# Performance work log

Measured on AMD Instinct MI355X. Metric: run time of the kernel, lower is better.

## Reference

```python
import jax, jax.numpy as jnp
import numpy as np
from itertools import product


def _gen_exps(num_vars, degree):
    return [e for e in product(range(degree + 1), repeat=num_vars) if sum(e) <= degree]

EXP_W = _gen_exps(7, 3)  # 120 terms
EXP_B = _gen_exps(3, 3)  # 20 terms
EXP_M = _gen_exps(5, 3)  # 56 terms (+1 diagonal coeff)


def _powers(x, exps):
    return {e: x ** e for e in exps}


def setup_inputs() -> dict:
    key = jax.random.key(0)
    ks = jax.random.split(key, 12)
    B, Din, Dout = 65536, 64, 64
    return {
        'x1': jax.random.normal(ks[0], (B, Din), jnp.float32),
        's1': jax.random.normal(ks[1], (B, Dout), jnp.float32),
        'y1': jax.random.normal(ks[2], (B, Dout), jnp.float32),
        'x2': jax.random.normal(ks[3], (B, Din), jnp.float32),
        's2': jax.random.normal(ks[4], (B, Dout), jnp.float32),
        'y2': jax.random.normal(ks[5], (B, Dout), jnp.float32),
        'w': jax.random.normal(ks[6], (Dout, Din), jnp.float32) * 0.1,
        'b': jax.random.normal(ks[7], (Dout,), jnp.float32) * 0.1,
        'm': jax.random.normal(ks[8], (Dout, Dout), jnp.float32) * 0.1,
        'params_w': jax.random.normal(ks[9], (len(EXP_W),), jnp.float32) * 0.1,
        'params_b': jax.random.normal(ks[10], (len(EXP_B),), jnp.float32) * 0.1,
        'params_m': jax.random.normal(ks[11], (len(EXP_M) + 1,), jnp.float32) * 0.1,
    }


def _dw(x1, s1, y1, x2, s2, y2, w, params_w):
    px1 = _powers(x1, {e[0] for e in EXP_W})
    ps1 = _powers(s1, {e[1] for e in EXP_W})
    py1 = _powers(y1, {e[2] for e in EXP_W})
    px2 = _powers(x2, {e[3] for e in EXP_W})
    ps2 = _powers(s2, {e[4] for e in EXP_W})
    py2 = _powers(y2, {e[5] for e in EXP_W})
    pw = _powers(w, {e[6] for e in EXP_W})
    inv_b = 1.0 / x1.shape[0]
    delta_w = jnp.zeros_like(w)
    for i, e in enumerate(EXP_W):
        y_term = ps1[e[1]] * py1[e[2]] * ps2[e[4]] * py2[e[5]]  # [B, Dout]
        x_term = px1[e[0]] * px2[e[3]]                          # [B, Din]
        delta_w = delta_w + (params_w[i] * inv_b) * (y_term.T @ x_term) * pw[e[6]]
    return delta_w  # bound=None (identity), l2_reg=0


def _db(y1, y2, b, params_b):
    py1 = _powers(y1, {e[0] for e in EXP_B})
    py2 = _powers(y2, {e[1] for e in EXP_B})
    pb = _powers(b, {e[2] for e in EXP_B})
    inv_b = 1.0 / y1.shape[0]
    delta_b = jnp.zeros_like(b)
    for i, e in enumerate(EXP_B):
        delta_b = delta_b + (params_b[i] * inv_b) * jnp.sum(py1[e[0]] * py2[e[1]], axis=0) * pb[e[2]]
    return delta_b


def _dm(y1, y2, m, params_m):
    ey1 = {e[0] for e in EXP_M} | {e[1] for e in EXP_M}
    ey2 = {e[2] for e in EXP_M} | {e[3] for e in EXP_M}
    py1 = _powers(y1, ey1)
    py2 = _powers(y2, ey2)
    pm = _powers(m, {e[4] for e in EXP_M})
    inv_b = 1.0 / y1.shape[0]
    delta_m = jnp.zeros_like(m)
    for i, e in enumerate(EXP_M):
        left = py1[e[1]] * py2[e[3]]   # [B, Dout]
        right = py1[e[0]] * py2[e[2]]  # [B, Dout]
        delta_m = delta_m + (params_m[i] * inv_b) * (left.T @ right) * pm[e[4]]
    delta_m = delta_m + params_m[-1] * jnp.eye(m.shape[0], dtype=m.dtype)
    return delta_m


def reference(x1, s1, y1, x2, s2, y2, w, b, m, params_w, params_b, params_m):
    delta_w = _dw(x1, s1, y1, x2, s2, y2, w, params_w)
    delta_b = _db(y1, y2, b, params_b)
    delta_m = _dm(y1, y2, m, params_m)
    return delta_w, delta_b, delta_m
```

## Files before the change

kernel.cpp:

```cpp
#include <hip/hip_runtime.h>
#include <type_traits>
#include <stdint.h>

#define DEV __device__ __forceinline__

typedef float f32x4 __attribute__((ext_vector_type(4)));
typedef short bf16x8 __attribute__((ext_vector_type(8)));
typedef unsigned short u16;
typedef u16 u16x4 __attribute__((ext_vector_type(4)));

static constexpr int BTOT = 65536;
static constexpr int KB   = 64;
static constexpr int NCHT = BTOT / KB;
static constexpr int NG   = 56;
static constexpr int NCOLSUM = 45;
static constexpr float INVB = 1.0f / (float)BTOT;

static constexpr int NWIN   = 64;
static constexpr int NBLK_C = 64;
static constexpr int NBLK_R = 256;
static constexpr int GRID   = 8*NWIN;

struct Col {
  int nslot, np, nsplit, nb;
  int8_t sexp[10][6];
  int8_t pa[16], pb[16];
  int16_t gout[16];
  uint8_t ldmask;
};

struct Tables {
  int nW, nB, nM, nA, nX;
  int8_t expw[120][7];
  int8_t expb[20][3];
  int8_t expm[56][5];
  int8_t am[35][4];
  int8_t xm[10][2];
  Col col[4];
  int8_t wtype[120]; int16_t widx[120]; int8_t wpow[120];
  int8_t mtype[56];  int16_t midx[56];  int8_t mpow[56];
  int16_t bcol[20];  int8_t bpow[20];
  int err, gcount;
};

constexpr int aidf(const Tables& t,int a,int b,int c,int d){
  for(int i=0;i<t.nA;i++)
    if(t.am[i][0]==a&&t.am[i][1]==b&&t.am[i][2]==c&&t.am[i][3]==d) return i;
  return -1;
}
constexpr int xidf(const Tables& t,int a,int b){
  for(int i=0;i<t.nX;i++) if(t.xm[i][0]==a&&t.xm[i][1]==b) return i;
  return -1;
}

constexpr Tables makeTables(){
  Tables t{};
  t.err = 0;
  t.nW=0;
  for(int e0=0;e0<4;e0++)for(int e1=0;e1<4;e1++)for(int e2=0;e2<4;e2++)
  for(int e3=0;e3<4;e3++)for(int e4=0;e4<4;e4++)for(int e5=0;e5<4;e5++)
  for(int e6=0;e6<4;e6++) if(e0+e1+e2+e3+e4+e5+e6<=3){
    t.expw[t.nW][0]=(int8_t)e0; t.expw[t.nW][1]=(int8_t)e1; t.expw[t.nW][2]=(int8_t)e2;
    t.expw[t.nW][3]=(int8_t)e3; t.expw[t.nW][4]=(int8_t)e4; t.expw[t.nW][5]=(int8_t)e5;
    t.expw[t.nW][6]=(int8_t)e6; t.nW++;
  }
  t.nB=0;
  for(int e0=0;e0<4;e0++)for(int e1=0;e1<4;e1++)for(int e2=0;e2<4;e2++)
    if(e0+e1+e2<=3){ t.expb[t.nB][0]=(int8_t)e0; t.expb[t.nB][1]=(int8_t)e1; t.expb[t.nB][2]=(int8_t)e2; t.nB++; }
  t.nM=0;
  for(int e0=0;e0<4;e0++)for(int e1=0;e1<4;e1++)for(int e2=0;e2<4;e2++)
  for(int e3=0;e3<4;e3++)for(int e4=0;e4<4;e4++)
    if(e0+e1+e2+e3+e4<=3){
      t.expm[t.nM][0]=(int8_t)e0; t.expm[t.nM][1]=(int8_t)e1; t.expm[t.nM][2]=(int8_t)e2;
      t.expm[t.nM][3]=(int8_t)e3; t.expm[t.nM][4]=(int8_t)e4; t.nM++;
    }
  t.nA=0;
  for(int a=0;a<4;a++)for(int b=0;b<4;b++)for(int c=0;c<4;c++)for(int d=0;d<4;d++)
    if(a+b+c+d<=3){ t.am[t.nA][0]=(int8_t)a; t.am[t.nA][1]=(int8_t)b; t.am[t.nA][2]=(int8_t)c; t.am[t.nA][3]=(int8_t)d; t.nA++; }
  t.nX=0;
  for(int a=0;a<4;a++)for(int b=0;b<4;b++)
    if(a+b<=3){ t.xm[t.nX][0]=(int8_t)a; t.xm[t.nX][1]=(int8_t)b; t.nX++; }

  int wslot[35][10]; int mslot[10][10];
  for(int i=0;i<35;i++)for(int j=0;j<10;j++) wslot[i][j]=-1;
  for(int i=0;i<10;i++)for(int j=0;j<10;j++) mslot[i][j]=-1;

  int slot=0;

  {
    Col& c = t.col[0]; c.nslot=5; c.nsplit=1; c.nb=NBLK_C;
    int ye[5][2] = {{0,1},{1,0},{0,2},{1,1},{2,0}};
    int xmid[5] = {0,0,0,0,0};
    for(int s=0;s<5;s++){
      c.sexp[s][0]=0; c.sexp[s][1]=(int8_t)ye[s][0]; c.sexp[s][2]=0;
      c.sexp[s][3]=(int8_t)ye[s][1]; c.sexp[s][4]=0; c.sexp[s][5]=0;
      xmid[s]=xidf(t, ye[s][0], ye[s][1]);
      if(xmid[s]<0) t.err+=1;
    }
    int p=0;
    for(int L=0;L<2;L++)for(int R=0;R<5;R++){
      c.pa[p]=(int8_t)L; c.pb[p]=(int8_t)R; c.gout[p]=(int16_t)slot;
      mslot[xmid[L]][xmid[R]]=slot; slot++; p++;
    }
    for(int L=2;L<5;L++)for(int R=0;R<2;R++){
      c.pa[p]=(int8_t)L; c.pb[p]=(int8_t)R; c.gout[p]=(int16_t)slot;
      mslot[xmid[L]][xmid[R]]=slot; slot++; p++;
    }
    c.np=p;
    if(p!=16) t.err+=1;
  }
  for(int wc=0; wc<2; wc++){
    Col& c = t.col[1+wc]; c.nslot=10; c.nsplit=1; c.nb=NBLK_C;
    int ae[5][2] = {{1,0},{0,1},{2,0},{1,1},{0,2}};
    int xe[5][2] = {{0,1},{1,0},{0,2},{1,1},{2,0}};
    int amid[5]={0,0,0,0,0}, xmidb[5]={0,0,0,0,0};
    for(int s=0;s<5;s++){
      for(int q=0;q<6;q++) c.sexp[s][q]=0;
      if(wc==0){ c.sexp[s][0]=(int8_t)ae[s][0]; c.sexp[s][1]=(int8_t)ae[s][1];
                 amid[s]=aidf(t, ae[s][0], ae[s][1], 0, 0); }
      else     { c.sexp[s][2]=(int8_t)ae[s][0]; c.sexp[s][3]=(int8_t)ae[s][1];
                 amid[s]=aidf(t, 0, 0, ae[s][0], ae[s][1]); }
      if(amid[s]<0) t.err+=1;
      for(int q=0;q<6;q++) c.sexp[5+s][q]=0;
      c.sexp[5+s][4]=(int8_t)xe[s][0]; c.sexp[5+s][5]=(int8_t)xe[s][1];
      xmidb[s]=xidf(t, xe[s][0], xe[s][1]);
      if(xmidb[s]<0) t.err+=1;
    }
    int p=0;
    for(int a=0;a<2;a++)for(int b=0;b<5;b++){
      c.pa[p]=(int8_t)a; c.pb[p]=(int8_t)(5+b); c.gout[p]=(int16_t)slot;
      wslot[amid[a]][xmidb[b]]=slot; slot++; p++;
    }
    for(int a=2;a<5;a++)for(int b=0;b<2;b++){
      c.pa[p]=(int8_t)a; c.pb[p]=(int8_t)(5+b); c.gout[p]=(int16_t)slot;
      wslot[amid[a]][xmidb[b]]=slot; slot++; p++;
    }
    c.np=p;
    if(p!=16) t.err+=1;
  }
  {
    Col& c = t.col[3]; c.nslot=6; c.nsplit=2; c.nb=NBLK_C;
    int ae4[4][4] = {{1,0,1,0},{1,0,0,1},{0,1,1,0},{0,1,0,1}};
    int xe[2][2] = {{0,1},{1,0}};
    int amid[4]={0,0,0,0}, xmidb[2]={0,0};
    for(int s=0;s<4;s++){
      c.sexp[s][0]=(int8_t)ae4[s][0]; c.sexp[s][1]=(int8_t)ae4[s][1];
      c.sexp[s][2]=(int8_t)ae4[s][2]; c.sexp[s][3]=(int8_t)ae4[s][3];
      c.sexp[s][4]=0; c.sexp[s][5]=0;
      amid[s]=aidf(t, ae4[s][0], ae4[s][1], ae4[s][2], ae4[s][3]);
      if(amid[s]<0) t.err+=1;
    }
    for(int s=0;s<2;s++){
      for(int q=0;q<6;q++) c.sexp[4+s][q]=0;
      c.sexp[4+s][4]=(int8_t)xe[s][0]; c.sexp[4+s][5]=(int8_t)xe[s][1];
      xmidb[s]=xidf(t, xe[s][0], xe[s][1]);
      if(xmidb[s]<0) t.err+=1;
    }
    int p=0;
    for(int a=0;a<4;a++)for(int b=0;b<2;b++){
      c.pa[p]=(int8_t)a; c.pb[p]=(int8_t)(4+b); c.gout[p]=(int16_t)slot;
      wslot[amid[a]][xmidb[b]]=slot; slot++; p++;
    }
    c.np=p;
    if(p!=8) t.err+=1;
  }
  t.gcount=slot;
  if(slot!=NG) t.err+=1;

  for(int ci=0; ci<4; ci++){
    unsigned m=0;
    for(int s=0;s<t.col[ci].nslot;s++)
      for(int v=0;v<6;v++) if(t.col[ci].sexp[s][v]>0) m |= (1u<<v);
    t.col[ci].ldmask=(uint8_t)m;
  }

  for(int i=0;i<t.nW;i++){
    const int8_t* e=t.expw[i];
    bool u0=(e[0]==0&&e[3]==0);
    bool v0=(e[1]==0&&e[2]==0&&e[4]==0&&e[5]==0);
    t.wpow[i]=e[6];
    if(u0){ t.wtype[i]=1; t.widx[i]=(int16_t)aidf(t,e[1],e[2],e[4],e[5]); }
    else if(v0){ t.wtype[i]=2; t.widx[i]=(int16_t)xidf(t,e[0],e[3]); }
    else {
      int s=wslot[aidf(t,e[1],e[2],e[4],e[5])][xidf(t,e[0],e[3])];
      if(s<0) t.err+=1;
      t.wtype[i]=0; t.widx[i]=(int16_t)s;
    }
  }
  for(int i=0;i<t.nM;i++){
    const int8_t* e=t.expm[i];
    bool L0=(e[1]==0&&e[3]==0), R0=(e[0]==0&&e[2]==0);
    t.mpow[i]=e[4];
    if(L0){ t.mtype[i]=2; t.midx[i]=(int16_t)aidf(t,0,e[0],0,e[2]); }
    else if(R0){ t.mtype[i]=1; t.midx[i]=(int16_t)aidf(t,0,e[1],0,e[3]); }
    else {
      int s=mslot[xidf(t,e[1],e[3])][xidf(t,e[0],e[2])];
      if(s<0) t.err+=1;
      t.mtype[i]=0; t.midx[i]=(int16_t)s;
    }
  }
  for(int i=0;i<t.nB;i++){
    const int8_t* e=t.expb[i];
    t.bcol[i]=(int16_t)aidf(t,0,e[0],0,e[1]); t.bpow[i]=e[2];
  }
  return t;
}

constexpr Tables TB = makeTables();
static_assert(TB.err==0 && TB.gcount==56, "table build failed");
static_assert(TB.nW==120 && TB.nB==20 && TB.nM==56 && TB.nA==35 && TB.nX==10, "enumeration mismatch");

template<int N, typename F>
DEV void sunroll(F&& f){
  if constexpr (N > 0){
    sunroll<N-1>(static_cast<F&&>(f));
    f(std::integral_constant<int, N-1>{});
  }
}
template<int E> DEV float ipw(float x){
  if constexpr(E==0) return 1.0f;
  else if constexpr(E==1) return x;
  else if constexpr(E==2) return x*x;
  else return x*x*x;
}
DEV u16 f2bf(float f){
  uint32_t u = __builtin_bit_cast(uint32_t, f);
  u = u + 0x7FFFu + ((u>>16)&1u);
  return (u16)(u>>16);
}

DEV bf16x8 readFrag(const u16* lds, int slot, int sb, int t, int l){
  return *(const bf16x8*)&lds[slot*4096 + ((sb*4 + t)*64 + l)*8];
}

template<int CI>
DEV void colGemm(const float* __restrict__ s1,const float* __restrict__ y1,
                 const float* __restrict__ s2,const float* __restrict__ y2,
                 const float* __restrict__ x1,const float* __restrict__ x2,
                 float* __restrict__ G, u16* lds, int tid, int bi)
{
  constexpr int NS  = TB.col[CI].nslot;
  constexpr int NSP = TB.col[CI].nsplit;
  constexpr int NDB = 4/NSP;
  constexpr int NB  = TB.col[CI].nb;
  constexpr unsigned LM = TB.col[CI].ldmask;

  const int l=tid&63, ob=(tid>>6)&3, sub=tid>>8, w=tid>>6;
  const int q = (l>>4)&3;
  const int ch = ob*16 + (l&15);
  const int bl = sub*16 + q*4;
  const int wbase = ((( (sub>>1)*4 + ob)*64) + ((sub&1)*2 + (q>>1))*16 + (l&15))*8 + (q&1)*4;

  int aslot=0,bslot=0,gsl=0,dbase=0;
  sunroll<16>([&](auto W){
    constexpr int ww = decltype(W)::value;
    if(w==ww){
      constexpr int p = ww/NSP;
      aslot = TB.col[CI].pa[p];
      bslot = TB.col[CI].pb[p];
      gsl   = TB.col[CI].gout[p];
      dbase = (ww%NSP)*2;
    }
  });

  const int c0 = (bi*NCHT)/NB, c1 = ((bi+1)*NCHT)/NB;
  f32x4 acc[4][NDB] = {};

  float raw[6][4] = {};
  float nraw[6][4] = {};

  auto issue = [&](int ck, float (&dst)[6][4]){
    const int b0 = (ck*KB + bl)*64 + ch;
    #pragma unroll
    for(int j=0;j<4;j++){
      const int off = b0 + j*64;
      if constexpr(LM&1u)  dst[0][j]=s1[off];
      if constexpr(LM&2u)  dst[1][j]=y1[off];
      if constexpr(LM&4u)  dst[2][j]=s2[off];
      if constexpr(LM&8u)  dst[3][j]=y2[off];
      if constexpr(LM&16u) dst[4][j]=x1[off];
      if constexpr(LM&32u) dst[5][j]=x2[off];
    }
  };

  issue(c0, raw);

  for(int ck=c0; ck<c1; ++ck){
    const int nk = (ck+1<c1)? ck+1 : c0;
    issue(nk, nraw);

    sunroll<NS>([&](auto S){
      constexpr int s = decltype(S)::value;
      u16x4 o4;
      #pragma unroll
      for(int j=0;j<4;j++){
        float v = ipw<TB.col[CI].sexp[s][0]>(raw[0][j])
                * ipw<TB.col[CI].sexp[s][1]>(raw[1][j])
                * ipw<TB.col[CI].sexp[s][2]>(raw[2][j])
                * ipw<TB.col[CI].sexp[s][3]>(raw[3][j])
                * ipw<TB.col[CI].sexp[s][4]>(raw[4][j])
                * ipw<TB.col[CI].sexp[s][5]>(raw[5][j]);
        o4[j]=f2bf(v);
      }
      *(u16x4*)&lds[s*4096 + wbase] = o4;
    });

    asm volatile("s_waitcnt lgkmcnt(0)" ::: "memory");
    __builtin_amdgcn_s_barrier();
    __builtin_amdgcn_sched_barrier(0);

    #pragma unroll
    for(int sb=0; sb<2; ++sb){
      bf16x8 Af[4];
      #pragma unroll
      for(int o2=0;o2<4;o2++) Af[o2]=readFrag(lds,aslot,sb,o2,l);
      #pragma unroll
      for(int dd=0;dd<NDB;dd++){
        bf16x8 Bf=readFrag(lds,bslot,sb,dbase+dd,l);
        #pragma unroll
        for(int o2=0;o2<4;o2++)
          acc[o2][dd]=__builtin_amdgcn_mfma_f32_16x16x32_bf16(Af[o2],Bf,acc[o2][dd],0,0,0);
      }
    }

    __builtin_amdgcn_sched_barrier(0);
    __builtin_amdgcn_s_barrier();
    __builtin_amdgcn_sched_barrier(0);

    #pragma unroll
    for(int a=0;a<6;a++)
      #pragma unroll
      for(int j=0;j<4;j++) raw[a][j]=nraw[a][j];
  }

  float* dst = G + gsl*4096;
  const int r0=(l>>4)*4, cc=l&15;
  #pragma unroll
  for(int o2=0;o2<4;o2++)
    #pragma unroll
    for(int dd=0;dd<NDB;dd++)
      #pragma unroll
      for(int r=0;r<4;r++)
        atomicAdd(&dst[(o2*16+r0+r)*64 + (dbase+dd)*16+cc], acc[o2][dd][r]);
}

DEV void colRed(const float* __restrict__ s1,const float* __restrict__ y1,
                const float* __restrict__ s2,const float* __restrict__ y2,
                const float* __restrict__ x1,const float* __restrict__ x2,
                float* __restrict__ col, float* ldsF, int tid, int bi)
{
  const int ch=tid&63, g=tid>>6;
  const int c0=(bi*NCHT)/NBLK_R, c1=((bi+1)*NCHT)/NBLK_R;
  float accv[45];
  sunroll<45>([&](auto K){ accv[decltype(K)::value]=0.f; });
  for(int r=c0*KB+g; r<c1*KB; r+=16){
    const int off=r*64+ch;
    const float v0=s1[off],v1=y1[off],v2=s2[off],v3=y2[off],v4=x1[off],v5=x2[off];
    sunroll<35>([&](auto K){
      constexpr int k=decltype(K)::value;
      accv[k] += ipw<TB.am[k][0]>(v0)*ipw<TB.am[k][1]>(v1)*ipw<TB.am[k][2]>(v2)*ipw<TB.am[k][3]>(v3);
    });
    sunroll<10>([&](auto K){
      constexpr int k=decltype(K)::value;
      accv[35+k] += ipw<TB.xm[k][0]>(v4)*ipw<TB.xm[k][1]>(v5);
    });
  }
  sunroll<5>([&](auto RR){
    constexpr int rr=decltype(RR)::value;
    __syncthreads();
    sunroll<9>([&](auto Q){
      constexpr int q=decltype(Q)::value;
      ldsF[(q*16+g)*64+ch]=accv[rr*9+q];
    });
    __syncthreads();
    if(tid<576){
      const int q=tid>>6, c=tid&63;
      float s=0.f;
      #pragma unroll
      for(int gg=0; gg<16; gg++) s+=ldsF[(q*16+gg)*64+c];
      atomicAdd(&col[(rr*9+q)*64+c], s);
    }
  });
}

__global__ __launch_bounds__(1024) void k_main(
    const float* __restrict__ x1, const float* __restrict__ s1, const float* __restrict__ y1,
    const float* __restrict__ x2, const float* __restrict__ s2, const float* __restrict__ y2,
    float* __restrict__ G, float* __restrict__ col)
{
  __shared__ u16 lds[10*4096];
  const int tid = threadIdx.x;
  const int u = blockIdx.x >> 6;
  const int g = blockIdx.x & 63;
  if      (u==0) colGemm<0>(s1,y1,s2,y2,x1,x2,G,lds,tid,g);
  else if (u==1) colGemm<1>(s1,y1,s2,y2,x1,x2,G,lds,tid,g);
  else if (u==2) colGemm<2>(s1,y1,s2,y2,x1,x2,G,lds,tid,g);
  else if (u==3) colGemm<3>(s1,y1,s2,y2,x1,x2,G,lds,tid,g);
  else           colRed(s1,y1,s2,y2,x1,x2,col,(float*)lds,tid, g*4 + (u-4));
}

__global__ __launch_bounds__(256) void k_combine(
    const float* __restrict__ G, const float* __restrict__ col,
    const float* __restrict__ w, const float* __restrict__ b, const float* __restrict__ m,
    const float* __restrict__ parw, const float* __restrict__ parb, const float* __restrict__ parm,
    float* __restrict__ out)
{
  const int n = blockIdx.x*256 + threadIdx.x;
  const int o = n>>6, d = n&63;
  const float wv = w[n], mv = m[n];
  const float wp[4] = {1.f, wv, wv*wv, wv*wv*wv};
  const float mp[4] = {1.f, mv, mv*mv, mv*mv*mv};
  float aw=0.f, am=0.f;
  sunroll<120>([&](auto II){
    constexpr int i = decltype(II)::value;
    constexpr int ty = TB.wtype[i];
    constexpr int ix = TB.widx[i];
    constexpr int q  = TB.wpow[i];
    float val;
    if constexpr(ty==0) val = G[ix*4096 + n];
    else if constexpr(ty==1) val = col[ix*64 + o];
    else val = col[(35+ix)*64 + d];
    aw += parw[i] * val * wp[q];
  });
  sunroll<56>([&](auto II){
    constexpr int i = decltype(II)::value;
    constexpr int ty = TB.mtype[i];
    constexpr int ix = TB.midx[i];
    constexpr int q  = TB.mpow[i];
    float val;
    if constexpr(ty==0) val = G[ix*4096 + n];
    else if constexpr(ty==1) val = col[ix*64 + o];
    else val = col[ix*64 + d];
    am += parm[i] * val * mp[q];
  });
  aw *= INVB; am *= INVB;
  if (o==d) am += parm[56];
  out[n] = aw;
  out[4160 + n] = am;
  if (n < 64){
    const float bv = b[n];
    const float bp[4] = {1.f, bv, bv*bv, bv*bv*bv};
    float ab=0.f;
    sunroll<20>([&](auto II){
      constexpr int i = decltype(II)::value;
      constexpr int cix = TB.bcol[i];
      constexpr int q = TB.bpow[i];
      ab += parb[i] * col[cix*64 + n] * bp[q];
    });
    out[4096 + n] = ab * INVB;
  }
}

extern "C" void kernel_launch(void* const* d_in, const int* in_sizes, int n_in,
                              void* d_out, int out_size, void* d_ws, size_t ws_size,
                              hipStream_t stream)
{
  const float* x1=(const float*)d_in[0];
  const float* s1=(const float*)d_in[1];
  const float* y1=(const float*)d_in[2];
  const float* x2=(const float*)d_in[3];
  const float* s2=(const float*)d_in[4];
  const float* y2=(const float*)d_in[5];
  const float* w =(const float*)d_in[6];
  const float* b =(const float*)d_in[7];
  const float* m =(const float*)d_in[8];
  const float* parw=(const float*)d_in[9];
  const float* parb=(const float*)d_in[10];
  const float* parm=(const float*)d_in[11];

  float* G   = (float*)d_ws;
  float* col = G + NG*4096;

  hipMemsetAsync(d_ws, 0, (size_t)(NG*4096 + NCOLSUM*64)*sizeof(float), stream);
  k_main<<<GRID, 1024, 0, stream>>>(x1,s1,y1,x2,s2,y2,G,col);
  k_combine<<<16, 256, 0, stream>>>(G,col,w,b,m,parw,parb,parm,(float*)d_out);
}
```

Baseline: 108.9 us.

## Halve block size and pair GEMM products per wave to reuse fragments

Blocks shrink from 1024 to 512 threads with two blocks per CU. Each wave now computes one or two full 64x64 products, grouped by a compile-time table so that the pair shares either its A or its B fragments, instead of splitting one product across waves. Each thread loads 8 rows and writes 8-wide bf16 vectors to LDS. The column-reduction blocks are resized to 8 row groups of 256 rows each. The aim is fewer redundant LDS fragment reads, wider stores, and better occupancy, at the cost of more accumulator registers per wave (two 4x4 f32x4 sets) and a possible spill risk under the 2-block launch bound.

```diff
diff --git a/kernel.cpp b/kernel.cpp
--- a/kernel.cpp
+++ b/kernel.cpp
@@ -7,7 +7,7 @@
 typedef float f32x4 __attribute__((ext_vector_type(4)));
 typedef short bf16x8 __attribute__((ext_vector_type(8)));
 typedef unsigned short u16;
-typedef u16 u16x4 __attribute__((ext_vector_type(4)));
+typedef u16 u16x8 __attribute__((ext_vector_type(8)));
 
 static constexpr int BTOT = 65536;
 static constexpr int KB   = 64;
@@ -19,7 +19,7 @@
 static constexpr int NWIN   = 64;
 static constexpr int NBLK_C = 64;
 static constexpr int NBLK_R = 256;
-static constexpr int GRID   = 8*NWIN;
+static constexpr int GRID   = 4*NWIN + NBLK_R;
 
 struct Col {
   int nslot, np, nsplit, nb;
@@ -210,6 +210,37 @@
 static_assert(TB.err==0 && TB.gcount==56, "table build failed");
 static_assert(TB.nW==120 && TB.nB==20 && TB.nM==56 && TB.nA==35 && TB.nX==10, "enumeration mismatch");
 
+constexpr int WP1[4][8] = {
+  {0,2,5,7,4,10,12,14},
+  {0,2,5,7,4,10,12,14},
+  {0,2,5,7,4,10,12,14},
+  {0,1,2,3,4,5,6,7}
+};
+constexpr int WP2[4][8] = {
+  {1,3,6,8,9,11,13,15},
+  {1,3,6,8,9,11,13,15},
+  {1,3,6,8,9,11,13,15},
+  {-1,-1,-1,-1,-1,-1,-1,-1}
+};
+constexpr bool wpOK(){
+  for(int c=0;c<4;c++){
+    bool used[16]={};
+    for(int w=0;w<8;w++){
+      int p1=WP1[c][w], p2=WP2[c][w];
+      if(p1<0||p1>=TB.col[c].np) return false;
+      if(used[p1]) return false; used[p1]=true;
+      if(p2>=0){
+        if(p2>=TB.col[c].np) return false;
+        if(used[p2]) return false; used[p2]=true;
+        if(TB.col[c].pa[p1]!=TB.col[c].pa[p2] && TB.col[c].pb[p1]!=TB.col[c].pb[p2]) return false;
+      }
+    }
+    for(int p=0;p<TB.col[c].np;p++) if(!used[p]) return false;
+  }
+  return true;
+}
+static_assert(wpOK(), "wave pair grouping invalid");
+
 template<int N, typename F>
 DEV void sunroll(F&& f){
   if constexpr (N > 0){
@@ -231,6 +262,10 @@
 
 DEV bf16x8 readFrag(const u16* lds, int slot, int sb, int t, int l){
   return *(const bf16x8*)&lds[slot*4096 + ((sb*4 + t)*64 + l)*8];
+}
+
+DEV f32x4 mfma_(bf16x8 a, bf16x8 b, f32x4 c){
+  return __builtin_amdgcn_mfma_f32_16x16x32_bf16(a, b, c, 0, 0, 0);
 }
 
 template<int CI>
@@ -239,40 +274,23 @@
                  const float* __restrict__ x1,const float* __restrict__ x2,
                  float* __restrict__ G, u16* lds, int tid, int bi)
 {
-  constexpr int NS  = TB.col[CI].nslot;
-  constexpr int NSP = TB.col[CI].nsplit;
-  constexpr int NDB = 4/NSP;
-  constexpr int NB  = TB.col[CI].nb;
+  constexpr int NS = TB.col[CI].nslot;
   constexpr unsigned LM = TB.col[CI].ldmask;
 
-  const int l=tid&63, ob=(tid>>6)&3, sub=tid>>8, w=tid>>6;
-  const int q = (l>>4)&3;
-  const int ch = ob*16 + (l&15);
-  const int bl = sub*16 + q*4;
-  const int wbase = ((( (sub>>1)*4 + ob)*64) + ((sub&1)*2 + (q>>1))*16 + (l&15))*8 + (q&1)*4;
-
-  int aslot=0,bslot=0,gsl=0,dbase=0;
-  sunroll<16>([&](auto W){
-    constexpr int ww = decltype(W)::value;
-    if(w==ww){
-      constexpr int p = ww/NSP;
-      aslot = TB.col[CI].pa[p];
-      bslot = TB.col[CI].pb[p];
-      gsl   = TB.col[CI].gout[p];
-      dbase = (ww%NSP)*2;
-    }
-  });
-
-  const int c0 = (bi*NCHT)/NB, c1 = ((bi+1)*NCHT)/NB;
-  f32x4 acc[4][NDB] = {};
-
-  float raw[6][4] = {};
-  float nraw[6][4] = {};
-
-  auto issue = [&](int ck, float (&dst)[6][4]){
-    const int b0 = (ck*KB + bl)*64 + ch;
+  const int l = tid&63, w = tid>>6;
+  const int wbase = (((w>>2)*4 + (l>>4))*64 + (w&3)*16 + (l&15))*8;
+
+  const int c0 = bi*16, c1 = c0+16;
+  f32x4 accA[4][4] = {};
+  f32x4 accB[4][4] = {};
+
+  float raw[6][8] = {};
+  float nraw[6][8] = {};
+
+  auto issue = [&](int ck, float (&dst)[6][8]){
+    const int b0 = (ck*KB + w*8)*64 + l;
     #pragma unroll
-    for(int j=0;j<4;j++){
+    for(int j=0;j<8;j++){
       const int off = b0 + j*64;
       if constexpr(LM&1u)  dst[0][j]=s1[off];
       if constexpr(LM&2u)  dst[1][j]=y1[off];
@@ -291,37 +309,73 @@
 
     sunroll<NS>([&](auto S){
       constexpr int s = decltype(S)::value;
-      u16x4 o4;
+      u16x8 o8;
       #pragma unroll
-      for(int j=0;j<4;j++){
+      for(int j=0;j<8;j++){
         float v = ipw<TB.col[CI].sexp[s][0]>(raw[0][j])
                 * ipw<TB.col[CI].sexp[s][1]>(raw[1][j])
                 * ipw<TB.col[CI].sexp[s][2]>(raw[2][j])
                 * ipw<TB.col[CI].sexp[s][3]>(raw[3][j])
                 * ipw<TB.col[CI].sexp[s][4]>(raw[4][j])
                 * ipw<TB.col[CI].sexp[s][5]>(raw[5][j]);
-        o4[j]=f2bf(v);
+        o8[j]=f2bf(v);
       }
-      *(u16x4*)&lds[s*4096 + wbase] = o4;
+      *(u16x8*)&lds[s*4096 + wbase] = o8;
     });
 
     asm volatile("s_waitcnt lgkmcnt(0)" ::: "memory");
     __builtin_amdgcn_s_barrier();
     __builtin_amdgcn_sched_barrier(0);
 
-    #pragma unroll
-    for(int sb=0; sb<2; ++sb){
-      bf16x8 Af[4];
-      #pragma unroll
-      for(int o2=0;o2<4;o2++) Af[o2]=readFrag(lds,aslot,sb,o2,l);
-      #pragma unroll
-      for(int dd=0;dd<NDB;dd++){
-        bf16x8 Bf=readFrag(lds,bslot,sb,dbase+dd,l);
+    sunroll<8>([&](auto WW){
+      constexpr int ww = decltype(WW)::value;
+      if(w==ww){
+        constexpr int P1 = WP1[CI][ww], P2 = WP2[CI][ww];
+        constexpr int SA1 = TB.col[CI].pa[P1], SB1 = TB.col[CI].pb[P1];
         #pragma unroll
-        for(int o2=0;o2<4;o2++)
-          acc[o2][dd]=__builtin_amdgcn_mfma_f32_16x16x32_bf16(Af[o2],Bf,acc[o2][dd],0,0,0);
+        for(int sb=0; sb<2; ++sb){
+          if constexpr(P2 >= 0){
+            constexpr int SA2 = TB.col[CI].pa[P2], SB2 = TB.col[CI].pb[P2];
+            if constexpr(SA1 == SA2){
+              bf16x8 Af[4];
+              #pragma unroll
+              for(int o2=0;o2<4;o2++) Af[o2]=readFrag(lds,SA1,sb,o2,l);
+              #pragma unroll
+              for(int dd=0;dd<4;dd++){
+                bf16x8 Bf1=readFrag(lds,SB1,sb,dd,l);
+                #pragma unroll
+                for(int o2=0;o2<4;o2++) accA[o2][dd]=mfma_(Af[o2],Bf1,accA[o2][dd]);
+                bf16x8 Bf2=readFrag(lds,SB2,sb,dd,l);
+                #pragma unroll
+                for(int o2=0;o2<4;o2++) accB[o2][dd]=mfma_(Af[o2],Bf2,accB[o2][dd]);
+              }
+            } else {
+              bf16x8 Af1[4], Af2[4];
+              #pragma unroll
+              for(int o2=0;o2<4;o2++){ Af1[o2]=readFrag(lds,SA1,sb,o2,l); Af2[o2]=readFrag(lds,SA2,sb,o2,l); }
+              #pragma unroll
+              for(int dd=0;dd<4;dd++){
+                bf16x8 Bf=readFrag(lds,SB1,sb,dd,l);
+                #pragma unroll
+                for(int o2=0;o2<4;o2++) accA[o2][dd]=mfma_(Af1[o2],Bf,accA[o2][dd]);
+                #pragma unroll
+                for(int o2=0;o2<4;o2++) accB[o2][dd]=mfma_(Af2[o2],Bf,accB[o2][dd]);
+              }
+            }
+          } else {
+            bf16x8 Af[4];
+            #pragma unroll
+            for(int o2=0;o2<4;o2++) Af[o2]=readFrag(lds,SA1,sb,o2,l);
+            #pragma unroll
+            for(int dd=0;dd<4;dd++){
+              bf16x8 Bf=readFrag(lds,SB1,sb,dd,l);
+              #pragma unroll
+              for(int o2=0;o2<4;o2++) accA[o2][dd]=mfma_(Af[o2],Bf,accA[o2][dd]);
+            }
+          }
+        }
       }
-    }
+    });
 
     __builtin_amdgcn_sched_barrier(0);
     __builtin_amdgcn_s_barrier();
@@ -330,18 +384,38 @@
     #pragma unroll
     for(int a=0;a<6;a++)
       #pragma unroll
-      for(int j=0;j<4;j++) raw[a][j]=nraw[a][j];
-  }
-
-  float* dst = G + gsl*4096;
+      for(int j=0;j<8;j++) raw[a][j]=nraw[a][j];
+  }
+
   const int r0=(l>>4)*4, cc=l&15;
-  #pragma unroll
-  for(int o2=0;o2<4;o2++)
-    #pragma unroll
-    for(int dd=0;dd<NDB;dd++)
-      #pragma unroll
-      for(int r=0;r<4;r++)
-        atomicAdd(&dst[(o2*16+r0+r)*64 + (dbase+dd)*16+cc], acc[o2][dd][r]);
+  sunroll<8>([&](auto WW){
+    constexpr int ww = decltype(WW)::value;
+    if(w==ww){
+      constexpr int P1 = WP1[CI][ww], P2 = WP2[CI][ww];
+      constexpr int G1 = TB.col[CI].gout[P1];
+      {
+        float* dst = G + G1*4096;
+        #pragma unroll
+        for(int o2=0;o2<4;o2++)
+          #pragma unroll
+          for(int dd=0;dd<4;dd++)
+            #pragma unroll
+            for(int r=0;r<4;r++)
+              atomicAdd(&dst[(o2*16+r0+r)*64 + dd*16+cc], accA[o2][dd][r]);
+      }
+      if constexpr(P2 >= 0){
+        constexpr int G2 = TB.col[CI].gout[P2];
+        float* dst = G + G2*4096;
+        #pragma unroll
+        for(int o2=0;o2<4;o2++)
+          #pragma unroll
+          for(int dd=0;dd<4;dd++)
+            #pragma unroll
+            for(int r=0;r<4;r++)
+              atomicAdd(&dst[(o2*16+r0+r)*64 + dd*16+cc], accB[o2][dd][r]);
+      }
+    }
+  });
 }
 
 DEV void colRed(const float* __restrict__ s1,const float* __restrict__ y1,
@@ -349,11 +423,11 @@
                 const float* __restrict__ x1,const float* __restrict__ x2,
                 float* __restrict__ col, float* ldsF, int tid, int bi)
 {
-  const int ch=tid&63, g=tid>>6;
-  const int c0=(bi*NCHT)/NBLK_R, c1=((bi+1)*NCHT)/NBLK_R;
+  const int ch=tid&63, g8=tid>>6;
+  const int row0 = bi*256;
   float accv[45];
   sunroll<45>([&](auto K){ accv[decltype(K)::value]=0.f; });
-  for(int r=c0*KB+g; r<c1*KB; r+=16){
+  for(int r=row0+g8; r<row0+256; r+=8){
     const int off=r*64+ch;
     const float v0=s1[off],v1=y1[off],v2=s2[off],v3=y2[off],v4=x1[off],v5=x2[off];
     sunroll<35>([&](auto K){
@@ -365,38 +439,46 @@
       accv[35+k] += ipw<TB.xm[k][0]>(v4)*ipw<TB.xm[k][1]>(v5);
     });
   }
-  sunroll<5>([&](auto RR){
+  sunroll<6>([&](auto RR){
     constexpr int rr=decltype(RR)::value;
     __syncthreads();
-    sunroll<9>([&](auto Q){
+    sunroll<8>([&](auto Q){
       constexpr int q=decltype(Q)::value;
-      ldsF[(q*16+g)*64+ch]=accv[rr*9+q];
+      if constexpr(rr*8+q < 45)
+        ldsF[(q*8+g8)*64+ch]=accv[rr*8+q];
     });
     __syncthreads();
-    if(tid<576){
-      const int q=tid>>6, c=tid&63;
-      float s=0.f;
-      #pragma unroll
-      for(int gg=0; gg<16; gg++) s+=ldsF[(q*16+gg)*64+c];
-      atomicAdd(&col[(rr*9+q)*64+c], s);
+    {
+      const int k=tid>>6, c=tid&63;
+      const int idx=rr*8+k;
+      if(idx<45){
+        float s=0.f;
+        #pragma unroll
+        for(int gg=0; gg<8; gg++) s+=ldsF[(k*8+gg)*64+c];
+        atomicAdd(&col[idx*64+c], s);
+      }
     }
   });
 }
 
-__global__ __launch_bounds__(1024) void k_main(
+__global__ __launch_bounds__(512, 2) void k_main(
     const float* __restrict__ x1, const float* __restrict__ s1, const float* __restrict__ y1,
     const float* __restrict__ x2, const float* __restrict__ s2, const float* __restrict__ y2,
     float* __restrict__ G, float* __restrict__ col)
 {
   __shared__ u16 lds[10*4096];
   const int tid = threadIdx.x;
-  const int u = blockIdx.x >> 6;
-  const int g = blockIdx.x & 63;
-  if      (u==0) colGemm<0>(s1,y1,s2,y2,x1,x2,G,lds,tid,g);
-  else if (u==1) colGemm<1>(s1,y1,s2,y2,x1,x2,G,lds,tid,g);
-  else if (u==2) colGemm<2>(s1,y1,s2,y2,x1,x2,G,lds,tid,g);
-  else if (u==3) colGemm<3>(s1,y1,s2,y2,x1,x2,G,lds,tid,g);
-  else           colRed(s1,y1,s2,y2,x1,x2,col,(float*)lds,tid, g*4 + (u-4));
+  const int bx = blockIdx.x;
+  if (bx < 4*NWIN){
+    const int u = bx >> 6;
+    const int g = bx & 63;
+    if      (u==0) colGemm<0>(s1,y1,s2,y2,x1,x2,G,lds,tid,g);
+    else if (u==1) colGemm<1>(s1,y1,s2,y2,x1,x2,G,lds,tid,g);
+    else if (u==2) colGemm<2>(s1,y1,s2,y2,x1,x2,G,lds,tid,g);
+    else           colGemm<3>(s1,y1,s2,y2,x1,x2,G,lds,tid,g);
+  } else {
+    colRed(s1,y1,s2,y2,x1,x2,col,(float*)lds,tid, bx - 4*NWIN);
+  }
 }
 
 __global__ __launch_bounds__(256) void k_combine(
@@ -472,6 +554,6 @@
   float* col = G + NG*4096;
 
   hipMemsetAsync(d_ws, 0, (size_t)(NG*4096 + NCOLSUM*64)*sizeof(float), stream);
-  k_main<<<GRID, 1024, 0, stream>>>(x1,s1,y1,x2,s2,y2,G,col);
+  k_main<<<GRID, 512, 0, stream>>>(x1,s1,y1,x2,s2,y2,G,col);
   k_combine<<<16, 256, 0, stream>>>(G,col,w,b,m,parw,parb,parm,(float*)d_out);
 }
```

New measurement: 114.7 us. 5.3% more time.

## Split Gram work into seven 8-product groups with double-buffered LDS pipeline

Applied to the files above, without the earlier changes.

Regroups the 56 Gram products into seven column groups of eight products each, with two waves per product, instead of four groups of up to sixteen. Each block now covers twice as many chunks. The GEMM loop double-buffers the bf16 power tiles in LDS so that staging the next chunk overlaps the MFMA work on the current one, which removes one barrier per iteration. It also resizes the grid to 32 windows, gives column-reduction blocks larger row ranges, and adds a launch-bounds occupancy hint, at the cost of fewer blocks and less parallelism per group.

```diff
diff --git a/kernel.cpp b/kernel.cpp
--- a/kernel.cpp
+++ b/kernel.cpp
@@ -16,16 +16,17 @@
 static constexpr int NCOLSUM = 45;
 static constexpr float INVB = 1.0f / (float)BTOT;
 
-static constexpr int NWIN   = 64;
-static constexpr int NBLK_C = 64;
-static constexpr int NBLK_R = 256;
-static constexpr int GRID   = 8*NWIN;
+static constexpr int NWIN  = 32;
+static constexpr int CHW   = NCHT / NWIN;
+static constexpr int NCOLG = 7;
+static constexpr int GRID  = 8*NWIN;
+static constexpr int BUFHALF = 8*4096;
 
 struct Col {
-  int nslot, np, nsplit, nb;
-  int8_t sexp[10][6];
-  int8_t pa[16], pb[16];
-  int16_t gout[16];
+  int nslot, np;
+  int8_t sexp[8][6];
+  int8_t pa[8], pb[8];
+  int16_t gout[8];
   uint8_t ldmask;
 };
 
@@ -36,7 +37,7 @@
   int8_t expm[56][5];
   int8_t am[35][4];
   int8_t xm[10][2];
-  Col col[4];
+  Col col[NCOLG];
   int8_t wtype[120]; int16_t widx[120]; int8_t wpow[120];
   int8_t mtype[56];  int16_t midx[56];  int8_t mpow[56];
   int16_t bcol[20];  int8_t bpow[20];
@@ -88,86 +89,90 @@
   int slot=0;
 
   {
-    Col& c = t.col[0]; c.nslot=5; c.nsplit=1; c.nb=NBLK_C;
-    int ye[5][2] = {{0,1},{1,0},{0,2},{1,1},{2,0}};
-    int xmid[5] = {0,0,0,0,0};
+    Col& c=t.col[0]; c.nslot=4; c.np=8;
+    int ym[4][2]={{0,1},{1,0},{0,2},{1,1}};
+    for(int s=0;s<4;s++){ for(int q=0;q<6;q++)c.sexp[s][q]=0;
+      c.sexp[s][1]=(int8_t)ym[s][0]; c.sexp[s][3]=(int8_t)ym[s][1]; }
+    int p=0;
+    for(int L=0;L<2;L++)for(int R=0;R<4;R++){
+      c.pa[p]=(int8_t)L; c.pb[p]=(int8_t)R; c.gout[p]=(int16_t)slot;
+      mslot[xidf(t,ym[L][0],ym[L][1])][xidf(t,ym[R][0],ym[R][1])]=slot; slot++; p++;
+    }
+  }
+  {
+    Col& c=t.col[1]; c.nslot=5; c.np=8;
+    int ym[5][2]={{0,1},{1,0},{0,2},{1,1},{2,0}};
+    for(int s=0;s<5;s++){ for(int q=0;q<6;q++)c.sexp[s][q]=0;
+      c.sexp[s][1]=(int8_t)ym[s][0]; c.sexp[s][3]=(int8_t)ym[s][1]; }
+    int p=0;
+    for(int L=0;L<2;L++){
+      c.pa[p]=(int8_t)L; c.pb[p]=4; c.gout[p]=(int16_t)slot;
+      mslot[xidf(t,ym[L][0],ym[L][1])][xidf(t,2,0)]=slot; slot++; p++;
+    }
+    for(int i=0;i<3;i++)for(int j=0;j<2;j++){
+      c.pa[p]=(int8_t)(2+i); c.pb[p]=(int8_t)j; c.gout[p]=(int16_t)slot;
+      mslot[xidf(t,ym[2+i][0],ym[2+i][1])][xidf(t,ym[j][0],ym[j][1])]=slot; slot++; p++;
+    }
+  }
+  for(int wc=0; wc<2; wc++){
+    Col& c=t.col[2+2*wc]; c.nslot=6; c.np=8;
+    int am2[2][2]={{1,0},{0,1}};
+    int xb[4][2]={{0,1},{1,0},{0,2},{1,1}};
+    for(int s=0;s<6;s++) for(int q=0;q<6;q++) c.sexp[s][q]=0;
+    for(int s=0;s<2;s++){
+      c.sexp[s][wc?2:0]=(int8_t)am2[s][0]; c.sexp[s][wc?3:1]=(int8_t)am2[s][1];
+    }
+    for(int s=0;s<4;s++){ c.sexp[2+s][4]=(int8_t)xb[s][0]; c.sexp[2+s][5]=(int8_t)xb[s][1]; }
+    int p=0;
+    for(int a=0;a<2;a++)for(int b=0;b<4;b++){
+      int amid = wc? aidf(t,0,0,am2[a][0],am2[a][1]) : aidf(t,am2[a][0],am2[a][1],0,0);
+      if(amid<0) t.err+=1;
+      c.pa[p]=(int8_t)a; c.pb[p]=(int8_t)(2+b); c.gout[p]=(int16_t)slot;
+      wslot[amid][xidf(t,xb[b][0],xb[b][1])]=slot; slot++; p++;
+    }
+  }
+  for(int wc=0; wc<2; wc++){
+    Col& c=t.col[3+2*wc]; c.nslot=8; c.np=8;
+    int am5[5][2]={{1,0},{0,1},{2,0},{1,1},{0,2}};
+    int xb[3][2]={{2,0},{0,1},{1,0}};
+    for(int s=0;s<8;s++) for(int q=0;q<6;q++) c.sexp[s][q]=0;
     for(int s=0;s<5;s++){
-      c.sexp[s][0]=0; c.sexp[s][1]=(int8_t)ye[s][0]; c.sexp[s][2]=0;
-      c.sexp[s][3]=(int8_t)ye[s][1]; c.sexp[s][4]=0; c.sexp[s][5]=0;
-      xmid[s]=xidf(t, ye[s][0], ye[s][1]);
-      if(xmid[s]<0) t.err+=1;
-    }
+      c.sexp[s][wc?2:0]=(int8_t)am5[s][0]; c.sexp[s][wc?3:1]=(int8_t)am5[s][1];
+    }
+    for(int s=0;s<3;s++){ c.sexp[5+s][4]=(int8_t)xb[s][0]; c.sexp[5+s][5]=(int8_t)xb[s][1]; }
     int p=0;
-    for(int L=0;L<2;L++)for(int R=0;R<5;R++){
-      c.pa[p]=(int8_t)L; c.pb[p]=(int8_t)R; c.gout[p]=(int16_t)slot;
-      mslot[xmid[L]][xmid[R]]=slot; slot++; p++;
-    }
-    for(int L=2;L<5;L++)for(int R=0;R<2;R++){
-      c.pa[p]=(int8_t)L; c.pb[p]=(int8_t)R; c.gout[p]=(int16_t)slot;
-      mslot[xmid[L]][xmid[R]]=slot; slot++; p++;
-    }
-    c.np=p;
-    if(p!=16) t.err+=1;
-  }
-  for(int wc=0; wc<2; wc++){
-    Col& c = t.col[1+wc]; c.nslot=10; c.nsplit=1; c.nb=NBLK_C;
-    int ae[5][2] = {{1,0},{0,1},{2,0},{1,1},{0,2}};
-    int xe[5][2] = {{0,1},{1,0},{0,2},{1,1},{2,0}};
-    int amid[5]={0,0,0,0,0}, xmidb[5]={0,0,0,0,0};
-    for(int s=0;s<5;s++){
-      for(int q=0;q<6;q++) c.sexp[s][q]=0;
-      if(wc==0){ c.sexp[s][0]=(int8_t)ae[s][0]; c.sexp[s][1]=(int8_t)ae[s][1];
-                 amid[s]=aidf(t, ae[s][0], ae[s][1], 0, 0); }
-      else     { c.sexp[s][2]=(int8_t)ae[s][0]; c.sexp[s][3]=(int8_t)ae[s][1];
-                 amid[s]=aidf(t, 0, 0, ae[s][0], ae[s][1]); }
-      if(amid[s]<0) t.err+=1;
-      for(int q=0;q<6;q++) c.sexp[5+s][q]=0;
-      c.sexp[5+s][4]=(int8_t)xe[s][0]; c.sexp[5+s][5]=(int8_t)xe[s][1];
-      xmidb[s]=xidf(t, xe[s][0], xe[s][1]);
-      if(xmidb[s]<0) t.err+=1;
-    }
-    int p=0;
-    for(int a=0;a<2;a++)for(int b=0;b<5;b++){
-      c.pa[p]=(int8_t)a; c.pb[p]=(int8_t)(5+b); c.gout[p]=(int16_t)slot;
-      wslot[amid[a]][xmidb[b]]=slot; slot++; p++;
-    }
-    for(int a=2;a<5;a++)for(int b=0;b<2;b++){
-      c.pa[p]=(int8_t)a; c.pb[p]=(int8_t)(5+b); c.gout[p]=(int16_t)slot;
-      wslot[amid[a]][xmidb[b]]=slot; slot++; p++;
-    }
-    c.np=p;
-    if(p!=16) t.err+=1;
+    for(int a=0;a<2;a++){
+      int amid = wc? aidf(t,0,0,am5[a][0],am5[a][1]) : aidf(t,am5[a][0],am5[a][1],0,0);
+      if(amid<0) t.err+=1;
+      c.pa[p]=(int8_t)a; c.pb[p]=5; c.gout[p]=(int16_t)slot;
+      wslot[amid][xidf(t,2,0)]=slot; slot++; p++;
+    }
+    for(int i=0;i<3;i++)for(int j=0;j<2;j++){
+      int amid = wc? aidf(t,0,0,am5[2+i][0],am5[2+i][1]) : aidf(t,am5[2+i][0],am5[2+i][1],0,0);
+      if(amid<0) t.err+=1;
+      c.pa[p]=(int8_t)(2+i); c.pb[p]=(int8_t)(6+j); c.gout[p]=(int16_t)slot;
+      wslot[amid][xidf(t,xb[1+j][0],xb[1+j][1])]=slot; slot++; p++;
+    }
   }
   {
-    Col& c = t.col[3]; c.nslot=6; c.nsplit=2; c.nb=NBLK_C;
-    int ae4[4][4] = {{1,0,1,0},{1,0,0,1},{0,1,1,0},{0,1,0,1}};
-    int xe[2][2] = {{0,1},{1,0}};
-    int amid[4]={0,0,0,0}, xmidb[2]={0,0};
-    for(int s=0;s<4;s++){
-      c.sexp[s][0]=(int8_t)ae4[s][0]; c.sexp[s][1]=(int8_t)ae4[s][1];
-      c.sexp[s][2]=(int8_t)ae4[s][2]; c.sexp[s][3]=(int8_t)ae4[s][3];
-      c.sexp[s][4]=0; c.sexp[s][5]=0;
-      amid[s]=aidf(t, ae4[s][0], ae4[s][1], ae4[s][2], ae4[s][3]);
-      if(amid[s]<0) t.err+=1;
-    }
-    for(int s=0;s<2;s++){
-      for(int q=0;q<6;q++) c.sexp[4+s][q]=0;
-      c.sexp[4+s][4]=(int8_t)xe[s][0]; c.sexp[4+s][5]=(int8_t)xe[s][1];
-      xmidb[s]=xidf(t, xe[s][0], xe[s][1]);
-      if(xmidb[s]<0) t.err+=1;
-    }
+    Col& c=t.col[6]; c.nslot=6; c.np=8;
+    int a4[4][4]={{1,0,1,0},{1,0,0,1},{0,1,1,0},{0,1,0,1}};
+    int xb[2][2]={{0,1},{1,0}};
+    for(int s=0;s<6;s++) for(int q=0;q<6;q++) c.sexp[s][q]=0;
+    for(int s=0;s<4;s++) for(int q=0;q<4;q++) c.sexp[s][q]=(int8_t)a4[s][q];
+    for(int s=0;s<2;s++){ c.sexp[4+s][4]=(int8_t)xb[s][0]; c.sexp[4+s][5]=(int8_t)xb[s][1]; }
     int p=0;
     for(int a=0;a<4;a++)for(int b=0;b<2;b++){
+      int amid = aidf(t,a4[a][0],a4[a][1],a4[a][2],a4[a][3]);
+      if(amid<0) t.err+=1;
       c.pa[p]=(int8_t)a; c.pb[p]=(int8_t)(4+b); c.gout[p]=(int16_t)slot;
-      wslot[amid[a]][xmidb[b]]=slot; slot++; p++;
-    }
-    c.np=p;
-    if(p!=8) t.err+=1;
+      wslot[amid][xidf(t,xb[b][0],xb[b][1])]=slot; slot++; p++;
+    }
   }
   t.gcount=slot;
   if(slot!=NG) t.err+=1;
 
-  for(int ci=0; ci<4; ci++){
+  for(int ci=0; ci<NCOLG; ci++){
     unsigned m=0;
     for(int s=0;s<t.col[ci].nslot;s++)
       for(int v=0;v<6;v++) if(t.col[ci].sexp[s][v]>0) m |= (1u<<v);
@@ -229,8 +234,11 @@
   return (u16)(u>>16);
 }
 
-DEV bf16x8 readFrag(const u16* lds, int slot, int sb, int t, int l){
-  return *(const bf16x8*)&lds[slot*4096 + ((sb*4 + t)*64 + l)*8];
+DEV bf16x8 readFrag(const u16* L, int slot, int sb, int tt, int l){
+  return *(const bf16x8*)&L[slot*4096 + ((sb*4 + tt)*64 + l)*8];
+}
+DEV f32x4 mfma_(bf16x8 a, bf16x8 b, f32x4 c){
+  return __builtin_amdgcn_mfma_f32_16x16x32_bf16(a, b, c, 0, 0, 0);
 }
 
 template<int CI>
@@ -239,109 +247,106 @@
                  const float* __restrict__ x1,const float* __restrict__ x2,
                  float* __restrict__ G, u16* lds, int tid, int bi)
 {
-  constexpr int NS  = TB.col[CI].nslot;
-  constexpr int NSP = TB.col[CI].nsplit;
-  constexpr int NDB = 4/NSP;
-  constexpr int NB  = TB.col[CI].nb;
+  constexpr int NS = TB.col[CI].nslot;
   constexpr unsigned LM = TB.col[CI].ldmask;
 
-  const int l=tid&63, ob=(tid>>6)&3, sub=tid>>8, w=tid>>6;
-  const int q = (l>>4)&3;
-  const int ch = ob*16 + (l&15);
-  const int bl = sub*16 + q*4;
-  const int wbase = ((( (sub>>1)*4 + ob)*64) + ((sub&1)*2 + (q>>1))*16 + (l&15))*8 + (q&1)*4;
-
-  int aslot=0,bslot=0,gsl=0,dbase=0;
-  sunroll<16>([&](auto W){
-    constexpr int ww = decltype(W)::value;
-    if(w==ww){
-      constexpr int p = ww/NSP;
-      aslot = TB.col[CI].pa[p];
-      bslot = TB.col[CI].pb[p];
-      gsl   = TB.col[CI].gout[p];
-      dbase = (ww%NSP)*2;
-    }
-  });
-
-  const int c0 = (bi*NCHT)/NB, c1 = ((bi+1)*NCHT)/NB;
-  f32x4 acc[4][NDB] = {};
-
-  float raw[6][4] = {};
-  float nraw[6][4] = {};
-
-  auto issue = [&](int ck, float (&dst)[6][4]){
-    const int b0 = (ck*KB + bl)*64 + ch;
+  const int l = tid&63, w = tid>>6;
+  const int wbase = ((w>>3)*4 + (l>>4))*512 + (((w>>1)&3)*16 + (l&15))*8 + (w&1)*4;
+
+  const int c0 = bi*CHW, c1 = c0+CHW;
+  f32x4 acc[4][2] = {};
+  float rw[6][4] = {};
+
+  auto issue = [&](int ck){
+    const int b0 = (ck*KB + w*4)*64 + l;
     #pragma unroll
     for(int j=0;j<4;j++){
       const int off = b0 + j*64;
-      if constexpr(LM&1u)  dst[0][j]=s1[off];
-      if constexpr(LM&2u)  dst[1][j]=y1[off];
-      if constexpr(LM&4u)  dst[2][j]=s2[off];
-      if constexpr(LM&8u)  dst[3][j]=y2[off];
-      if constexpr(LM&16u) dst[4][j]=x1[off];
-      if constexpr(LM&32u) dst[5][j]=x2[off];
+      if constexpr(LM&1u)  rw[0][j]=s1[off];
+      if constexpr(LM&2u)  rw[1][j]=y1[off];
+      if constexpr(LM&4u)  rw[2][j]=s2[off];
+      if constexpr(LM&8u)  rw[3][j]=y2[off];
+      if constexpr(LM&16u) rw[4][j]=x1[off];
+      if constexpr(LM&32u) rw[5][j]=x2[off];
     }
   };
-
-  issue(c0, raw);
-
-  for(int ck=c0; ck<c1; ++ck){
-    const int nk = (ck+1<c1)? ck+1 : c0;
-    issue(nk, nraw);
-
+  auto stage = [&](int buf){
+    u16* L = lds + buf*BUFHALF;
     sunroll<NS>([&](auto S){
       constexpr int s = decltype(S)::value;
       u16x4 o4;
       #pragma unroll
       for(int j=0;j<4;j++){
-        float v = ipw<TB.col[CI].sexp[s][0]>(raw[0][j])
-                * ipw<TB.col[CI].sexp[s][1]>(raw[1][j])
-                * ipw<TB.col[CI].sexp[s][2]>(raw[2][j])
-                * ipw<TB.col[CI].sexp[s][3]>(raw[3][j])
-                * ipw<TB.col[CI].sexp[s][4]>(raw[4][j])
-                * ipw<TB.col[CI].sexp[s][5]>(raw[5][j]);
+        float v = ipw<TB.col[CI].sexp[s][0]>(rw[0][j])
+                * ipw<TB.col[CI].sexp[s][1]>(rw[1][j])
+                * ipw<TB.col[CI].sexp[s][2]>(rw[2][j])
+                * ipw<TB.col[CI].sexp[s][3]>(rw[3][j])
+                * ipw<TB.col[CI].sexp[s][4]>(rw[4][j])
+                * ipw<TB.col[CI].sexp[s][5]>(rw[5][j]);
         o4[j]=f2bf(v);
       }
-      *(u16x4*)&lds[s*4096 + wbase] = o4;
-    });
+      *(u16x4*)&L[s*4096 + wbase] = o4;
+    });
+  };
+
+  issue(c0);
+  stage(0);
+  asm volatile("s_waitcnt lgkmcnt(0)" ::: "memory");
+  __builtin_amdgcn_s_barrier();
+  __builtin_amdgcn_sched_barrier(0);
+
+  for(int k=c0; k<c1; ++k){
+    const int t = k - c0;
+    const bool notlast = (k+1 < c1);
+    if(notlast) issue(k+1);
+
+    const u16* L = lds + (t&1)*BUFHALF;
+    sunroll<16>([&](auto WW){
+      constexpr int ww = decltype(WW)::value;
+      if(w==ww){
+        constexpr int p  = ww>>1;
+        constexpr int SA = TB.col[CI].pa[p];
+        constexpr int SB = TB.col[CI].pb[p];
+        constexpr int DB = (ww&1)*2;
+        #pragma unroll
+        for(int sb=0; sb<2; ++sb){
+          bf16x8 Af[4];
+          #pragma unroll
+          for(int o2=0;o2<4;o2++) Af[o2]=readFrag(L,SA,sb,o2,l);
+          #pragma unroll
+          for(int dd=0;dd<2;dd++){
+            bf16x8 Bf=readFrag(L,SB,sb,DB+dd,l);
+            #pragma unroll
+            for(int o2=0;o2<4;o2++) acc[o2][dd]=mfma_(Af[o2],Bf,acc[o2][dd]);
+          }
+        }
+      }
+    });
+
+    if(notlast) stage((t+1)&1);
 
     asm volatile("s_waitcnt lgkmcnt(0)" ::: "memory");
     __builtin_amdgcn_s_barrier();
     __builtin_amdgcn_sched_barrier(0);
-
-    #pragma unroll
-    for(int sb=0; sb<2; ++sb){
-      bf16x8 Af[4];
+  }
+
+  const int r0=(l>>4)*4, cc=l&15;
+  sunroll<16>([&](auto WW){
+    constexpr int ww = decltype(WW)::value;
+    if(w==ww){
+      constexpr int p  = ww>>1;
+      constexpr int GS = TB.col[CI].gout[p];
+      constexpr int DB = (ww&1)*2;
+      float* dst = G + GS*4096;
       #pragma unroll
-      for(int o2=0;o2<4;o2++) Af[o2]=readFrag(lds,aslot,sb,o2,l);
-      #pragma unroll
-      for(int dd=0;dd<NDB;dd++){
-        bf16x8 Bf=readFrag(lds,bslot,sb,dbase+dd,l);
+      for(int o2=0;o2<4;o2++)
         #pragma unroll
-        for(int o2=0;o2<4;o2++)
-          acc[o2][dd]=__builtin_amdgcn_mfma_f32_16x16x32_bf16(Af[o2],Bf,acc[o2][dd],0,0,0);
-      }
-    }
-
-    __builtin_amdgcn_sched_barrier(0);
-    __builtin_amdgcn_s_barrier();
-    __builtin_amdgcn_sched_barrier(0);
-
-    #pragma unroll
-    for(int a=0;a<6;a++)
-      #pragma unroll
-      for(int j=0;j<4;j++) raw[a][j]=nraw[a][j];
-  }
-
-  float* dst = G + gsl*4096;
-  const int r0=(l>>4)*4, cc=l&15;
-  #pragma unroll
-  for(int o2=0;o2<4;o2++)
-    #pragma unroll
-    for(int dd=0;dd<NDB;dd++)
-      #pragma unroll
-      for(int r=0;r<4;r++)
-        atomicAdd(&dst[(o2*16+r0+r)*64 + (dbase+dd)*16+cc], acc[o2][dd][r]);
+        for(int dd=0;dd<2;dd++)
+          #pragma unroll
+          for(int r=0;r<4;r++)
+            atomicAdd(&dst[(o2*16+r0+r)*64 + (DB+dd)*16+cc], acc[o2][dd][r]);
+    }
+  });
 }
 
 DEV void colRed(const float* __restrict__ s1,const float* __restrict__ y1,
@@ -349,11 +354,11 @@
                 const float* __restrict__ x1,const float* __restrict__ x2,
                 float* __restrict__ col, float* ldsF, int tid, int bi)
 {
-  const int ch=tid&63, g=tid>>6;
-  const int c0=(bi*NCHT)/NBLK_R, c1=((bi+1)*NCHT)/NBLK_R;
+  const int ch=tid&63, g16=tid>>6;
+  const int base = bi*2048;
   float accv[45];
   sunroll<45>([&](auto K){ accv[decltype(K)::value]=0.f; });
-  for(int r=c0*KB+g; r<c1*KB; r+=16){
+  for(int r=base+g16; r<base+2048; r+=16){
     const int off=r*64+ch;
     const float v0=s1[off],v1=y1[off],v2=s2[off],v3=y2[off],v4=x1[off],v5=x2[off];
     sunroll<35>([&](auto K){
@@ -365,38 +370,45 @@
       accv[35+k] += ipw<TB.xm[k][0]>(v4)*ipw<TB.xm[k][1]>(v5);
     });
   }
-  sunroll<5>([&](auto RR){
+  sunroll<6>([&](auto RR){
     constexpr int rr=decltype(RR)::value;
     __syncthreads();
-    sunroll<9>([&](auto Q){
+    sunroll<8>([&](auto Q){
       constexpr int q=decltype(Q)::value;
-      ldsF[(q*16+g)*64+ch]=accv[rr*9+q];
+      if constexpr(rr*8+q < 45)
+        ldsF[(q*16+g16)*64+ch]=accv[rr*8+q];
     });
     __syncthreads();
-    if(tid<576){
-      const int q=tid>>6, c=tid&63;
-      float s=0.f;
-      #pragma unroll
-      for(int gg=0; gg<16; gg++) s+=ldsF[(q*16+gg)*64+c];
-      atomicAdd(&col[(rr*9+q)*64+c], s);
+    {
+      const int k=tid>>6, c=tid&63;
+      const int idx=rr*8+k;
+      if(k<8 && idx<45){
+        float s=0.f;
+        #pragma unroll
+        for(int gg=0; gg<16; gg++) s+=ldsF[(k*16+gg)*64+c];
+        atomicAdd(&col[idx*64+c], s);
+      }
     }
   });
 }
 
-__global__ __launch_bounds__(1024) void k_main(
+__global__ __launch_bounds__(1024, 4) void k_main(
     const float* __restrict__ x1, const float* __restrict__ s1, const float* __restrict__ y1,
     const float* __restrict__ x2, const float* __restrict__ s2, const float* __restrict__ y2,
     float* __restrict__ G, float* __restrict__ col)
 {
-  __shared__ u16 lds[10*4096];
+  __shared__ u16 lds[2*BUFHALF];
   const int tid = threadIdx.x;
-  const int u = blockIdx.x >> 6;
-  const int g = blockIdx.x & 63;
+  const int u = blockIdx.x >> 5;
+  const int g = blockIdx.x & 31;
   if      (u==0) colGemm<0>(s1,y1,s2,y2,x1,x2,G,lds,tid,g);
   else if (u==1) colGemm<1>(s1,y1,s2,y2,x1,x2,G,lds,tid,g);
   else if (u==2) colGemm<2>(s1,y1,s2,y2,x1,x2,G,lds,tid,g);
   else if (u==3) colGemm<3>(s1,y1,s2,y2,x1,x2,G,lds,tid,g);
-  else           colRed(s1,y1,s2,y2,x1,x2,col,(float*)lds,tid, g*4 + (u-4));
+  else if (u==4) colGemm<4>(s1,y1,s2,y2,x1,x2,G,lds,tid,g);
+  else if (u==5) colGemm<5>(s1,y1,s2,y2,x1,x2,G,lds,tid,g);
+  else if (u==6) colGemm<6>(s1,y1,s2,y2,x1,x2,G,lds,tid,g);
+  else           colRed(s1,y1,s2,y2,x1,x2,col,(float*)lds,tid,g);
 }
 
 __global__ __launch_bounds__(256) void k_combine(
```

New measurement: 97.11 us. 10.9% less time.
